# Kernel optimization log

Measured on AMD Instinct MI355X. Metric: run time of the kernel, lower is better.

## Reference

```python
import jax, jax.numpy as jnp
import numpy as np

K, N, M, D = 64, 8192, 8, 32  # locations, time steps, covariate features, memory depth


def setup_inputs() -> dict:
    key = jax.random.key(0)
    ks = jax.random.split(key, 6)
    obs = jax.random.uniform(ks[0], (K, N), dtype=jnp.float32)            # event counts [K, N]
    covs = jax.random.normal(ks[1], (K, N, M), dtype=jnp.float32)          # covariates  [K, N, M]
    hbeta = jnp.array([2.0], dtype=jnp.float32)                            # decay rate param (torch init: 2)
    halpha = jax.random.uniform(ks[2], (K, K), dtype=jnp.float32) * 0.01   # excitation matrix, U(0, 0.01)
    gamma = jax.random.uniform(ks[3], (K,), dtype=jnp.float32) * 0.01      # covariate gate, U(0, 0.01)
    W1 = jax.random.normal(ks[4], (20, 2 * D * M), dtype=jnp.float32) * 0.05
    b1 = jnp.zeros((20,), dtype=jnp.float32)
    W2 = jax.random.normal(ks[5], (1, 20), dtype=jnp.float32) * 0.05
    b2 = jnp.zeros((1,), dtype=jnp.float32)
    return dict(obs=obs, covs=covs, hbeta=hbeta, halpha=halpha, gamma=gamma,
                W1=W1, b1=b1, W2=W2, b2=b2)


def _forward(obs, covs, hbeta, halpha, gamma, W1, b1, W2, b2):
    k, n = obs.shape
    beta = hbeta[0]
    decay = jnp.exp(-beta)

    # Excitation: S[t] = sum_{tp < t} obs[:, tp] * beta * exp(-(t - tp) * beta)
    # exact O(N) linear recurrence instead of the original per-t O(t) resummation.
    def step(S, o):
        return decay * (S + beta * o), S
    _, S_all = jax.lax.scan(step, jnp.zeros((k,), obs.dtype), obs.T)  # [N, K]
    lam1 = jax.nn.softplus(jnp.einsum('kj,nj->kn', halpha, S_all))     # [K, N] (hmu = 0 in subclass)

    # Edge-padded covariate windows: window at t is padded[:, t : t + 2D, :]
    padded = jnp.concatenate([
        jnp.repeat(covs[:, :1, :], D, axis=1),   # left pad with first step
        covs,
        jnp.repeat(covs[:, -1:, :], D, axis=1),  # right pad with last step
    ], axis=1)                                   # [K, N + 2D, M]
    idx = jnp.arange(n)[:, None] + jnp.arange(2 * D)[None, :]  # [N, 2D]
    X = padded[:, idx, :].reshape(k, n, 2 * D * M)             # [K, N, 2DM], time-major then M (matches torch reshape)

    # Tiny 2-layer MLP with softplus activations, vectorized over (K, N)
    h = jax.nn.softplus(jnp.einsum('knf,hf->knh', X, W1) + b1)           # [K, N, 20]
    mu = jax.nn.softplus(jnp.einsum('knh,oh->kno', h, W2) + b2)[..., 0]  # [K, N]

    lams = lam1 + gamma[:, None] * mu                                    # [K, N]
    loglik = jnp.sum(obs * jnp.log(lams) - lams)
    return loglik, lams


def reference(obs, covs, hbeta, halpha, gamma, W1, b1, W2, b2):
    return _forward(obs, covs, hbeta, halpha, gamma, W1, b1, W2, b2)
```

## Files before the change

### kernel.cpp

```cpp
#include <hip/hip_runtime.h>
#include <hip/hip_bf16.h>
#include <math.h>

#define KL 64
#define NT 8192
#define MF 8
#define DD 32
#define WIN 64
#define HD 20
#define HP 32
#define KF 512
#define BS 1024
#define WPB 16
#define NCOLS (WPB * 64)
#define GX (NT / NCOLS)
#define NBLK (GX * KL)
#define NPART (NBLK * WPB)
#define GRPS (KF / 8)
#define GROW 24
#define W1SZ (GRPS * GROW * 8)

typedef __attribute__((ext_vector_type(8))) short bf16x8;
typedef __attribute__((ext_vector_type(4))) float f32x4;
typedef __attribute__((ext_vector_type(4))) unsigned u32x4;

__device__ __forceinline__ float softplus_f(float x) {
    float e = __expf(-fabsf(x));
    return fmaxf(x, 0.0f) + __logf(1.0f + e);
}
__device__ __forceinline__ short f2bf(float x) {
    __hip_bfloat16 h = __float2bfloat16(x);
    return *reinterpret_cast<short*>(&h);
}
__device__ __forceinline__ unsigned pkbf(float a, float b) {
    unsigned r;
    asm("v_cvt_pk_bf16_f32 %0, %1, %2" : "=v"(r) : "v"(a), "v"(b));
    return r;
}

__global__ __launch_bounds__(256)
void pack_kernel(const float* __restrict__ W1, const float* __restrict__ b1,
                 const float* __restrict__ W2, const float* __restrict__ hbeta,
                 short* __restrict__ W1b, float* __restrict__ b1p,
                 float* __restrict__ W2p, float* __restrict__ wtab) {
    int t = blockIdx.x * 256 + threadIdx.x;
    #pragma unroll
    for (int i = 0; i < 3; ++i) {
        int p = t + i * 4096;
        int e = p & 7;
        int rg = p >> 3;
        int r = rg % GROW;
        int grp = rg / GROW;
        W1b[p] = (r < HD) ? f2bf(W1[r * KF + grp * 8 + e]) : (short)0;
    }
    if (blockIdx.x == 0 && threadIdx.x < HP) {
        b1p[threadIdx.x] = (threadIdx.x < HD) ? b1[threadIdx.x] : 0.0f;
        W2p[threadIdx.x] = (threadIdx.x < HD) ? W2[threadIdx.x] : 0.0f;
    }
    if (blockIdx.x == 0 && threadIdx.x < WIN) {
        float bt = hbeta[0];
        wtab[threadIdx.x] = bt * __expf(-bt * (float)(threadIdx.x + 1));
    }
}

__global__ __launch_bounds__(BS)
void mlp_mfma_kernel(const float* __restrict__ covs, const float* __restrict__ obs,
                     const float* __restrict__ halpha, const float* __restrict__ hbeta,
                     const short* __restrict__ W1b, const float* __restrict__ b1p,
                     const float* __restrict__ W2p, const float* __restrict__ b2,
                     const float* __restrict__ gamma, const float* __restrict__ wt,
                     float* __restrict__ lams, float* __restrict__ partial) {
    __shared__ short cov_s[WPB][128 * MF];
    __shared__ float T_s[NCOLS + WIN];

    int k    = blockIdx.y;
    int N0   = blockIdx.x * NCOLS;
    int tid  = threadIdx.x;
    int lane = tid & 63;
    int wave = tid >> 6;
    int base = N0 + wave * 64;

    int n = base + lane;
    size_t idx = (size_t)k * NT + n;
    float obs_n = obs[idx];
    float beta  = hbeta[0];
    float gam   = gamma[k];
    float b2v   = b2[0];

    const float* cbase = covs + (size_t)k * NT * MF;
    {
        int t1 = base - DD + lane;
        t1 = t1 < 0 ? 0 : t1;
        int t2 = base + DD + lane;
        t2 = t2 > NT - 1 ? NT - 1 : t2;
        const float4* cp1 = (const float4*)(cbase + (size_t)t1 * MF);
        const float4* cp2 = (const float4*)(cbase + (size_t)t2 * MF);
        float4 a0 = cp1[0], a1 = cp1[1];
        float4 d0 = cp2[0], d1 = cp2[1];
        u32x4 q1 = { pkbf(a0.x, a0.y), pkbf(a0.z, a0.w),
                     pkbf(a1.x, a1.y), pkbf(a1.z, a1.w) };
        u32x4 q2 = { pkbf(d0.x, d0.y), pkbf(d0.z, d0.w),
                     pkbf(d1.x, d1.y), pkbf(d1.z, d1.w) };
        *(u32x4*)&cov_s[wave][lane * MF] = q1;
        *(u32x4*)&cov_s[wave][(lane + 64) * MF] = q2;
    }

    int c = lane & 15;
    int g = lane >> 4;

    f32x4 acc[4][2];
    #pragma unroll
    for (int mt = 0; mt < 4; ++mt) {
        acc[mt][0] = (f32x4){0.f, 0.f, 0.f, 0.f};
        acc[mt][1] = (f32x4){0.f, 0.f, 0.f, 0.f};
    }

    int r1 = (c < 4) ? (16 + c) : HD;
    const short* pB0 = W1b + g * (GROW * 8) + c * 8;
    const short* pB1 = W1b + g * (GROW * 8) + r1 * 8;
    const short* pA  = &cov_s[wave][(c + g) * MF];

    const float* arow = halpha + (size_t)k * KL;
    int tA = base - WIN + lane;
    tA = tA < 0 ? 0 : tA;
    int tB = base + lane;
    float aA = 0.0f, aB = 0.0f;

    #pragma unroll 2
    for (int kk = 0; kk < KF / 32; ++kk) {
        #pragma unroll
        for (int jj = 0; jj < 4; ++jj) {
            int j = kk * 4 + jj;
            aA = fmaf(arow[j], (obs + (size_t)j * NT)[tA], aA);
        }
        if (wave == WPB - 1) {
            #pragma unroll
            for (int jj = 0; jj < 4; ++jj) {
                int j = kk * 4 + jj;
                aB = fmaf(arow[j], (obs + (size_t)j * NT)[tB], aB);
            }
        }
        bf16x8 b0  = *(const bf16x8*)(pB0 + kk * (4 * GROW * 8));
        bf16x8 b1v = *(const bf16x8*)(pB1 + kk * (4 * GROW * 8));
        #pragma unroll
        for (int mt = 0; mt < 4; ++mt) {
            bf16x8 a = *(const bf16x8*)(pA + (mt * 16 + kk * 4) * MF);
            acc[mt][0] = __builtin_amdgcn_mfma_f32_16x16x32_bf16(a, b0,  acc[mt][0], 0, 0, 0);
            acc[mt][1] = __builtin_amdgcn_mfma_f32_16x16x32_bf16(a, b1v, acc[mt][1], 0, 0, 0);
        }
    }
    T_s[wave * 64 + lane] = aA;
    if (wave == WPB - 1) T_s[NCOLS + lane] = aB;
    __syncthreads();

    float w2a = W2p[c],      b1a = b1p[c];
    float w2b = W2p[16 + c], b1b = b1p[16 + c];
    float cur[16];
    #pragma unroll
    for (int mt = 0; mt < 4; ++mt) {
        #pragma unroll
        for (int j = 0; j < 4; ++j) {
            cur[mt * 4 + j] = w2a * softplus_f(acc[mt][0][j] + b1a)
                            + w2b * softplus_f(acc[mt][1][j] + b1b);
        }
    }
    #pragma unroll
    for (int m = 1; m <= 8; m <<= 1) {
        int half = 8 / m;
        #pragma unroll
        for (int s = 0; s < half; ++s) {
            float x0 = cur[s], x1 = cur[s + half];
            float t = (lane & m) ? x0 : x1;
            float u = __shfl_xor(t, m, 64);
            cur[s] = ((lane & m) ? x1 : x0) + u;
        }
    }
    float pre;
    {
        int mt_ = lane >> 4, gg = (lane >> 2) & 3, jj_ = lane & 3;
        int iv2 = (mt_ << 2) | jj_;
        int src = gg * 16 + (((iv2 & 1) << 3) | ((iv2 & 2) << 1) |
                             ((iv2 & 4) >> 1) | ((iv2 & 8) >> 3));
        pre = __shfl(cur[0], src, 64);
    }

    const float* Tp = &T_s[64 + wave * 64 + lane];
    float la = 0.0f;
    if (base >= WIN && beta >= 1.6667f) {
        float la0 = 0.f, la1 = 0.f, la2 = 0.f, la3 = 0.f;
        #pragma unroll
        for (int it = 0; it < 5; ++it) {
            la0 = fmaf(wt[4 * it + 0], Tp[-(4 * it + 1)], la0);
            la1 = fmaf(wt[4 * it + 1], Tp[-(4 * it + 2)], la1);
            la2 = fmaf(wt[4 * it + 2], Tp[-(4 * it + 3)], la2);
            la3 = fmaf(wt[4 * it + 3], Tp[-(4 * it + 4)], la3);
        }
        la = (la0 + la1) + (la2 + la3);
    } else {
        float decay = __expf(-beta);
        int Lmax = (int)(30.0f / beta) + 2;
        if (Lmax > WIN) Lmax = WIN;
        float w = beta * decay;
        for (int i = 1; i <= Lmax; ++i) {
            if (i <= n) la = fmaf(w, Tp[-i], la);
            w *= decay;
        }
    }
    float lam1 = softplus_f(la);
    float mu = softplus_f(pre + b2v);
    float lam = lam1 + gam * mu;
    lams[idx] = lam;
    float term = fmaf(obs_n, __logf(lam), -lam);

    #pragma unroll
    for (int off = 32; off > 0; off >>= 1) term += __shfl_down(term, off, 64);
    if (lane == 0)
        partial[((size_t)blockIdx.y * GX + blockIdx.x) * WPB + wave] = term;
}

__global__ __launch_bounds__(256)
void finalize_kernel(const float* __restrict__ partial, float* __restrict__ out0) {
    __shared__ float wred[4];
    int tid = threadIdx.x;
    float s = 0.0f;
    #pragma unroll
    for (int i = 0; i < NPART / 256; ++i) s += partial[i * 256 + tid];
    #pragma unroll
    for (int off = 32; off > 0; off >>= 1) s += __shfl_down(s, off, 64);
    if ((tid & 63) == 0) wred[tid >> 6] = s;
    __syncthreads();
    if (tid == 0) out0[0] = (wred[0] + wred[1]) + (wred[2] + wred[3]);
}

extern "C" void kernel_launch(void* const* d_in, const int* in_sizes, int n_in,
                              void* d_out, int out_size, void* d_ws, size_t ws_size,
                              hipStream_t stream) {
    const float* obs    = (const float*)d_in[0];
    const float* covs   = (const float*)d_in[1];
    const float* hbeta  = (const float*)d_in[2];
    const float* halpha = (const float*)d_in[3];
    const float* gamma  = (const float*)d_in[4];
    const float* W1     = (const float*)d_in[5];
    const float* b1     = (const float*)d_in[6];
    const float* W2     = (const float*)d_in[7];
    const float* b2     = (const float*)d_in[8];

    float* out  = (float*)d_out;
    float* lams = out + 1;

    char* ws = (char*)d_ws;
    float* partial = (float*)ws;
    float* b1p     = (float*)(ws + 32768);
    float* W2p     = (float*)(ws + 32896);
    float* wtab    = (float*)(ws + 33024);
    short* W1b     = (short*)(ws + 33280);

    pack_kernel<<<dim3(16), dim3(256), 0, stream>>>(W1, b1, W2, hbeta,
                                                    W1b, b1p, W2p, wtab);
    mlp_mfma_kernel<<<dim3(GX, KL), dim3(BS), 0, stream>>>(
        covs, obs, halpha, hbeta, W1b, b1p, W2p, b2, gamma, wtab, lams, partial);
    finalize_kernel<<<1, dim3(256), 0, stream>>>(partial, out);
}
```

Baseline: 43.45 us.

## Switch window MLP to 32x32x16 bf16 MFMA with remapped output rows

Replaces the eight 16x16x32 MFMAs per k-step with two 32x32x16 MFMAs that cover the 20 hidden units, padded to 32, in one N tile. W1 is repacked into a matching B layout, and each lane's output time index is remapped so the cross-lane reduction leaves the result in place and the final shuffle goes away. This cuts padding waste on the hidden dimension (20 padded to 32 instead of two 16-wide tiles) and reduces per-step LDS A-fragment loads. The cost is a larger accumulator footprint and a more complex lane-to-row mapping.

```diff
diff --git a/kernel.cpp b/kernel.cpp
--- a/kernel.cpp
+++ b/kernel.cpp
@@ -16,12 +16,10 @@
 #define GX (NT / NCOLS)
 #define NBLK (GX * KL)
 #define NPART (NBLK * WPB)
-#define GRPS (KF / 8)
-#define GROW 24
-#define W1SZ (GRPS * GROW * 8)
+#define BPSZ (64 * 32 * 8)
 
 typedef __attribute__((ext_vector_type(8))) short bf16x8;
-typedef __attribute__((ext_vector_type(4))) float f32x4;
+typedef __attribute__((ext_vector_type(16))) float f32x16;
 typedef __attribute__((ext_vector_type(4))) unsigned u32x4;
 
 __device__ __forceinline__ float softplus_f(float x) {
@@ -41,17 +39,17 @@
 __global__ __launch_bounds__(256)
 void pack_kernel(const float* __restrict__ W1, const float* __restrict__ b1,
                  const float* __restrict__ W2, const float* __restrict__ hbeta,
-                 short* __restrict__ W1b, float* __restrict__ b1p,
+                 short* __restrict__ Bp, float* __restrict__ b1p,
                  float* __restrict__ W2p, float* __restrict__ wtab) {
     int t = blockIdx.x * 256 + threadIdx.x;
     #pragma unroll
-    for (int i = 0; i < 3; ++i) {
+    for (int i = 0; i < 4; ++i) {
         int p = t + i * 4096;
-        int e = p & 7;
-        int rg = p >> 3;
-        int r = rg % GROW;
-        int grp = rg / GROW;
-        W1b[p] = (r < HD) ? f2bf(W1[r * KF + grp * 8 + e]) : (short)0;
+        int m = p & 7;
+        int dc = p >> 3;
+        int col = dc & 31;
+        int d = dc >> 5;
+        Bp[p] = (col < HD) ? f2bf(W1[col * KF + d * 8 + m]) : (short)0;
     }
     if (blockIdx.x == 0 && threadIdx.x < HP) {
         b1p[threadIdx.x] = (threadIdx.x < HD) ? b1[threadIdx.x] : 0.0f;
@@ -66,7 +64,7 @@
 __global__ __launch_bounds__(BS)
 void mlp_mfma_kernel(const float* __restrict__ covs, const float* __restrict__ obs,
                      const float* __restrict__ halpha, const float* __restrict__ hbeta,
-                     const short* __restrict__ W1b, const float* __restrict__ b1p,
+                     const short* __restrict__ Bp, const float* __restrict__ b1p,
                      const float* __restrict__ W2p, const float* __restrict__ b2,
                      const float* __restrict__ gamma, const float* __restrict__ wt,
                      float* __restrict__ lams, float* __restrict__ partial) {
@@ -80,7 +78,12 @@
     int wave = tid >> 6;
     int base = N0 + wave * 64;
 
-    int n = base + lane;
+    int v  = ((lane & 1) << 4) | ((lane & 2) << 2) | (lane & 4) |
+             ((lane & 8) >> 2) | ((lane & 16) >> 4);
+    int rg = v & 15;
+    int rm = ((v >> 4) << 5) + (rg & 3) + ((rg >> 2) << 3) + ((lane >> 5) << 2);
+
+    int n = base + rm;
     size_t idx = (size_t)k * NT + n;
     float obs_n = obs[idx];
     float beta  = hbeta[0];
@@ -105,20 +108,10 @@
         *(u32x4*)&cov_s[wave][(lane + 64) * MF] = q2;
     }
 
-    int c = lane & 15;
-    int g = lane >> 4;
-
-    f32x4 acc[4][2];
-    #pragma unroll
-    for (int mt = 0; mt < 4; ++mt) {
-        acc[mt][0] = (f32x4){0.f, 0.f, 0.f, 0.f};
-        acc[mt][1] = (f32x4){0.f, 0.f, 0.f, 0.f};
-    }
-
-    int r1 = (c < 4) ? (16 + c) : HD;
-    const short* pB0 = W1b + g * (GROW * 8) + c * 8;
-    const short* pB1 = W1b + g * (GROW * 8) + r1 * 8;
-    const short* pA  = &cov_s[wave][(c + g) * MF];
+    f32x16 acc0 = {0.f}, acc1 = {0.f};
+
+    const short* pA = &cov_s[wave][((lane & 31) + (lane >> 5)) * MF];
+    const short* pB = Bp + (((lane >> 5) << 5) + (lane & 31)) * 8;
 
     const float* arow = halpha + (size_t)k * KL;
     int tA = base - WIN + lane;
@@ -127,64 +120,50 @@
     float aA = 0.0f, aB = 0.0f;
 
     #pragma unroll 2
-    for (int kk = 0; kk < KF / 32; ++kk) {
+    for (int kk = 0; kk < 32; ++kk) {
         #pragma unroll
-        for (int jj = 0; jj < 4; ++jj) {
-            int j = kk * 4 + jj;
+        for (int jj = 0; jj < 2; ++jj) {
+            int j = kk * 2 + jj;
             aA = fmaf(arow[j], (obs + (size_t)j * NT)[tA], aA);
         }
         if (wave == WPB - 1) {
             #pragma unroll
-            for (int jj = 0; jj < 4; ++jj) {
-                int j = kk * 4 + jj;
+            for (int jj = 0; jj < 2; ++jj) {
+                int j = kk * 2 + jj;
                 aB = fmaf(arow[j], (obs + (size_t)j * NT)[tB], aB);
             }
         }
-        bf16x8 b0  = *(const bf16x8*)(pB0 + kk * (4 * GROW * 8));
-        bf16x8 b1v = *(const bf16x8*)(pB1 + kk * (4 * GROW * 8));
-        #pragma unroll
-        for (int mt = 0; mt < 4; ++mt) {
-            bf16x8 a = *(const bf16x8*)(pA + (mt * 16 + kk * 4) * MF);
-            acc[mt][0] = __builtin_amdgcn_mfma_f32_16x16x32_bf16(a, b0,  acc[mt][0], 0, 0, 0);
-            acc[mt][1] = __builtin_amdgcn_mfma_f32_16x16x32_bf16(a, b1v, acc[mt][1], 0, 0, 0);
-        }
+        bf16x8 b  = *(const bf16x8*)(pB + kk * 512);
+        bf16x8 a0 = *(const bf16x8*)(pA + (2 * kk) * MF);
+        bf16x8 a1 = *(const bf16x8*)(pA + (32 + 2 * kk) * MF);
+        acc0 = __builtin_amdgcn_mfma_f32_32x32x16_bf16(a0, b, acc0, 0, 0, 0);
+        acc1 = __builtin_amdgcn_mfma_f32_32x32x16_bf16(a1, b, acc1, 0, 0, 0);
     }
     T_s[wave * 64 + lane] = aA;
     if (wave == WPB - 1) T_s[NCOLS + lane] = aB;
     __syncthreads();
 
-    float w2a = W2p[c],      b1a = b1p[c];
-    float w2b = W2p[16 + c], b1b = b1p[16 + c];
-    float cur[16];
-    #pragma unroll
-    for (int mt = 0; mt < 4; ++mt) {
-        #pragma unroll
-        for (int j = 0; j < 4; ++j) {
-            cur[mt * 4 + j] = w2a * softplus_f(acc[mt][0][j] + b1a)
-                            + w2b * softplus_f(acc[mt][1][j] + b1b);
-        }
-    }
-    #pragma unroll
-    for (int m = 1; m <= 8; m <<= 1) {
-        int half = 8 / m;
+    float w2a = W2p[lane & 31];
+    float b1a = b1p[lane & 31];
+    float cur[32];
+    #pragma unroll
+    for (int r = 0; r < 16; ++r) cur[r]      = w2a * softplus_f(acc0[r] + b1a);
+    #pragma unroll
+    for (int r = 0; r < 16; ++r) cur[16 + r] = w2a * softplus_f(acc1[r] + b1a);
+    #pragma unroll
+    for (int m = 1; m <= 16; m <<= 1) {
+        int half = 16 / m;
         #pragma unroll
         for (int s = 0; s < half; ++s) {
             float x0 = cur[s], x1 = cur[s + half];
-            float t = (lane & m) ? x0 : x1;
-            float u = __shfl_xor(t, m, 64);
+            float tsel = (lane & m) ? x0 : x1;
+            float u = __shfl_xor(tsel, m, 64);
             cur[s] = ((lane & m) ? x1 : x0) + u;
         }
     }
-    float pre;
-    {
-        int mt_ = lane >> 4, gg = (lane >> 2) & 3, jj_ = lane & 3;
-        int iv2 = (mt_ << 2) | jj_;
-        int src = gg * 16 + (((iv2 & 1) << 3) | ((iv2 & 2) << 1) |
-                             ((iv2 & 4) >> 1) | ((iv2 & 8) >> 3));
-        pre = __shfl(cur[0], src, 64);
-    }
-
-    const float* Tp = &T_s[64 + wave * 64 + lane];
+    float pre = cur[0];
+
+    const float* Tp = &T_s[64 + wave * 64 + rm];
     float la = 0.0f;
     if (base >= WIN && beta >= 1.6667f) {
         float la0 = 0.f, la1 = 0.f, la2 = 0.f, la3 = 0.f;
@@ -253,11 +232,11 @@
     float* b1p     = (float*)(ws + 32768);
     float* W2p     = (float*)(ws + 32896);
     float* wtab    = (float*)(ws + 33024);
-    short* W1b     = (short*)(ws + 33280);
+    short* Bp      = (short*)(ws + 33280);
 
     pack_kernel<<<dim3(16), dim3(256), 0, stream>>>(W1, b1, W2, hbeta,
-                                                    W1b, b1p, W2p, wtab);
+                                                    Bp, b1p, W2p, wtab);
     mlp_mfma_kernel<<<dim3(GX, KL), dim3(BS), 0, stream>>>(
-        covs, obs, halpha, hbeta, W1b, b1p, W2p, b2, gamma, wtab, lams, partial);
+        covs, obs, halpha, hbeta, Bp, b1p, W2p, b2, gamma, wtab, lams, partial);
     finalize_kernel<<<1, dim3(256), 0, stream>>>(partial, out);
 }
```

Result: slower. 53.66 us (+23.5%).
